# Kernel tuning notes

Hardware: AMD Instinct MI355X
Metric: run time of the kernel (lower is better)

The kernel has to match this reference:

```python
import jax, jax.numpy as jnp
import numpy as np

B, N, E = 64, 512, 262144
D_EMB = 128   # 2 * embedding_dim
D_H = 128     # residue_emb_dim == iegmn_lay_hid_dim
L = 5         # iegmn_n_lays
X_INIT = 0.25 # residual mix toward original coords (IEGMN x_connection_init)


def silu(x):
    return x * jax.nn.sigmoid(x)


def _edges(k):
    # within-graph random edges: pick a graph, then a node inside it
    g = jax.random.randint(k, (E,), 0, B)
    n = jax.random.randint(jax.random.fold_in(k, 1), (E,), 0, N)
    return (g * N + n).astype(jnp.int32)


def setup_inputs() -> dict:
    key = jax.random.key(0)
    ks = jax.random.split(key, 16)
    Nt = B * N
    s = 0.05
    feat = jax.random.normal(ks[0], (Nt, D_EMB), jnp.float32)
    coords = jax.random.normal(ks[1], (Nt, 3), jnp.float32)
    c_valid = (jax.random.uniform(ks[2], (B, N)) > 0.3).astype(jnp.float32)
    c_valid = c_valid.at[:, 0].set(1.0)  # avoid empty graphs
    return {
        'feat': feat,
        'coords': coords,
        'c_valid': c_valid,
        'edge_src': _edges(ks[3]), 'edge_dst': _edges(ks[4]),
        'cross_src': _edges(ks[5]), 'cross_dst': _edges(ks[6]),
        'W_emb': jax.random.normal(ks[7], (D_H, D_EMB), jnp.float32) * s,
        'We1': jax.random.normal(ks[8], (L, 2 * D_H + 1, D_H), jnp.float32) * s,
        'be1': jnp.zeros((L, D_H), jnp.float32),
        'We2': jax.random.normal(ks[9], (L, D_H, D_H), jnp.float32) * s,
        'be2': jnp.zeros((L, D_H), jnp.float32),
        'Wx': jax.random.normal(ks[10], (L, D_H, 1), jnp.float32) * s,
        'Wh': jax.random.normal(ks[11], (L, 3 * D_H, D_H), jnp.float32) * s,
        'bh': jnp.zeros((L, D_H), jnp.float32),
        'Wfc': jax.random.normal(ks[12], (3, D_H, D_H), jnp.float32) * s,
        'bfc': jnp.zeros((3, D_H), jnp.float32),
        'Wout': jax.random.normal(ks[13], (D_H, 1), jnp.float32) * s,
        'bout': jnp.zeros((1,), jnp.float32),
    }


def _deg_inv(dst, n):
    deg = jax.ops.segment_sum(jnp.ones(dst.shape[0], jnp.float32), dst, num_segments=n)
    return (1.0 / jnp.maximum(deg, 1.0))[:, None]


def _iegmn_layer(p, src, dst, x, h, x0, h0, deg_inv):
    We1, be1, We2, be2, Wx, Wh, bh = p
    n = x.shape[0]
    dx = x[src] - x[dst]                                  # [E, 3]
    d2 = jnp.sum(dx * dx, -1, keepdims=True)              # [E, 1]
    m = silu(jnp.concatenate([h[src], h[dst], d2], -1) @ We1 + be1)
    m = silu(m @ We2 + be2)                               # [E, D_H]
    coef = jnp.tanh(m @ Wx)                               # [E, 1]
    agg_x = jax.ops.segment_sum(dx * coef, dst, num_segments=n) * deg_inv
    x_new = X_INIT * x0 + (1.0 - X_INIT) * x + agg_x
    agg_m = jax.ops.segment_sum(m, dst, num_segments=n) * deg_inv
    h_new = silu(jnp.concatenate([h, agg_m, h0], -1) @ Wh + bh)
    return x_new, h_new


def reference(feat, coords, c_valid, edge_src, edge_dst, cross_src, cross_dst,
              W_emb, We1, be1, We2, be2, Wx, Wh, bh, Wfc, bfc, Wout, bout):
    Nt = feat.shape[0]
    h = feat @ W_emb.T          # embede (no bias)
    h0, x0, x = h, coords, coords
    dgi = _deg_inv(edge_dst, Nt)
    dci = _deg_inv(cross_dst, Nt)
    for k in range(L):
        p = tuple(t[k] for t in (We1, be1, We2, be2, Wx, Wh, bh))
        # branch == 'both': run layer on graph then cross_graph with same input h
        x, c1 = _iegmn_layer(p, edge_src, edge_dst, x, h, x0, h0, dgi)
        x, c2 = _iegmn_layer(p, cross_src, cross_dst, x, h, x0, h0, dci)
        h = c2 - c1             # dropout is identity at inference
    # masked sum-pool / count
    hb = h.reshape(B, N, D_H)
    pooled = jnp.sum(hb * c_valid[..., None], axis=1) / jnp.sum(c_valid, axis=1, keepdims=True)
    z = pooled
    for i in range(Wfc.shape[0]):
        z = jax.nn.relu(z @ Wfc[i] + bfc[i])
    out = jax.nn.sigmoid(z @ Wout + bout)
    return out.reshape(-1)      # [B]
```

## Files before the change

### kernel.cpp

```cpp
#include <hip/hip_runtime.h>

#define DEVINL __device__ __forceinline__

constexpr int NT   = 32768;
constexpr int DH   = 128;
constexpr int NE   = 262144;
constexpr int BGR  = 64;
constexpr int NPG  = 512;
constexpr int LAYS = 5;
constexpr size_t LSTR = 32768*3 + 98304;

typedef __attribute__((ext_vector_type(8))) short bf16x8;
typedef __attribute__((ext_vector_type(4))) float f32x4;
typedef __attribute__((ext_vector_type(4))) unsigned int uint4v;
typedef unsigned int uint;

DEVINL float siluf(float v){ return v * (1.0f/(1.0f + __expf(-v))); }
DEVINL float tanh_fast(float x){ float e = __expf(2.0f*x); return 1.0f - 2.0f/(e + 1.0f); }

DEVINL uint bf16_rne(float f){
  uint x = __float_as_uint(f);
  return (x + 0x7fffu + ((x>>16)&1u)) >> 16;
}

DEVINL void split8(const float* m, bf16x8& h, bf16x8& l){
  #pragma unroll
  for (int j=0;j<8;j++){
    uint x  = __float_as_uint(m[j]);
    uint hb = x >> 16;
    float hf = __uint_as_float(hb<<16);
    uint lb = bf16_rne(m[j] - hf);
    h[j] = (short)hb; l[j] = (short)lb;
  }
}

DEVINL f32x4 mma3(bf16x8 ah, bf16x8 al, bf16x8 bh, bf16x8 bl, f32x4 acc){
  acc = __builtin_amdgcn_mfma_f32_16x16x32_bf16(al, bh, acc, 0,0,0);
  acc = __builtin_amdgcn_mfma_f32_16x16x32_bf16(ah, bl, acc, 0,0,0);
  acc = __builtin_amdgcn_mfma_f32_16x16x32_bf16(ah, bh, acc, 0,0,0);
  return acc;
}

__global__ __launch_bounds__(256) void k_prep_all(
    const float* __restrict__ W_emb, const float* __restrict__ We1,
    const float* __restrict__ We2,  const float* __restrict__ Wh,
    short* __restrict__ wemb_p, short* __restrict__ lay_p)
{
  const int idx = blockIdx.x*256 + threadIdx.x;
  const float* src; short* dst; int v; bool trans = false;
  if (idx < 16384){ src = W_emb; dst = wemb_p; v = idx; trans = true; }
  else {
    const int u = idx - 16384;
    const int layer = u / 98304;
    const int w = u - layer*98304;
    short* p = lay_p + (size_t)layer*LSTR;
    if (w < 16384)      { src = We1 + (size_t)layer*257*DH;          dst = p;         v = w; }
    else if (w < 32768) { src = We1 + (size_t)layer*257*DH + 128*DH; dst = p + 32768; v = w - 16384; }
    else if (w < 49152) { src = We2 + (size_t)layer*DH*DH;           dst = p + 65536; v = w - 32768; }
    else                { src = Wh  + (size_t)layer*3*DH*DH;         dst = p + 98304; v = w - 49152; }
  }
  const int k = v>>7, col = v&127;
  const float val = trans ? src[(size_t)col*128 + k] : src[(size_t)k*128 + col];
  uint hb = __float_as_uint(val) >> 16;
  float hf = __uint_as_float(hb<<16);
  uint lb = bf16_rne(val - hf);
  const int kc = k>>5, q = (k&31)>>3, j = k&7;
  const size_t o = (size_t)kc*8192 + q*1024 + col*8 + j;
  dst[o]        = (short)hb;
  dst[o + 4096] = (short)lb;
}

__global__ __launch_bounds__(256) void k_hist2(const int* __restrict__ edst,
                                               const int* __restrict__ cdst,
                                               int* __restrict__ cnt){
  const int half = blockIdx.x >= (NE/256);
  const int e = (blockIdx.x - half*(NE/256))*256 + threadIdx.x;
  const int* d = half ? cdst : edst;
  atomicAdd(&cnt[half*NT + d[e]], 1);
}

__global__ __launch_bounds__(1024) void k_scan2(const int* __restrict__ cnt,
                                                int* __restrict__ cur,
                                                float* __restrict__ dinv){
  __shared__ int part[1024];
  const int off = blockIdx.x * NT;
  const int tid = threadIdx.x;
  const int base = tid*32;
  int s = 0;
  for (int i=0;i<32;i++){
    const int c = cnt[off + base + i];
    dinv[off + base + i] = 1.0f / (float)(c > 1 ? c : 1);
    s += c;
  }
  const int own = s;
  part[tid] = s; __syncthreads();
  for (int o=1; o<1024; o<<=1){
    int v = (tid>=o) ? part[tid-o] : 0;
    __syncthreads();
    part[tid] += v;
    __syncthreads();
  }
  int run = part[tid] - own;
  for (int i=0;i<32;i++){ cur[off + base + i] = run; run += cnt[off + base + i]; }
}

__global__ __launch_bounds__(256) void k_scatter2(const int* __restrict__ edst,
                                                  const int* __restrict__ cdst,
                                                  int* __restrict__ cur,
                                                  int* __restrict__ perm){
  const int half = blockIdx.x >= (NE/256);
  const int e = (blockIdx.x - half*(NE/256))*256 + threadIdx.x;
  const int* d = half ? cdst : edst;
  const int p = atomicAdd(&cur[half*NT + d[e]], 1);
  perm[half*NE + p] = e;
}

template<int MODE>
__global__ __launch_bounds__(512) void k_ngemm(
    const float* __restrict__ A0, float* __restrict__ A1, const float* __restrict__ A2,
    const float* __restrict__ dinv, const short* __restrict__ W0, const short* __restrict__ W1,
    const float* __restrict__ bias, const float* __restrict__ c1in,
    float* __restrict__ out0, float* __restrict__ out1)
{
  const int tid = threadIdx.x;
  const int wv = tid>>6, lane = tid&63, c = lane&15, q = lane>>4;
  const int rowt = wv & 3, grp = wv >> 2;
  const int row = blockIdx.x*64 + rowt*16 + c;
  constexpr int KC = (MODE>=2) ? 12 : 4;
  constexpr int TT = (MODE==1) ? 8 : 4;
  float dv = 1.0f;
  if constexpr (MODE>=2) dv = dinv[row];
  const short* Wp = W0;
  if constexpr (MODE==1){ if (grp==1) Wp = W1; }
  f32x4 acc[TT];
  #pragma unroll
  for (int t=0;t<TT;t++){ acc[t][0]=0.f; acc[t][1]=0.f; acc[t][2]=0.f; acc[t][3]=0.f; }

  #pragma unroll
  for (int kc=0; kc<KC; ++kc){
    const float* asrc = A0; float sc = 1.0f;
    if constexpr (MODE>=2){
      if (kc >= 8)      { asrc = A2; }
      else if (kc >= 4) { asrc = A1; sc = dv; }
    }
    const int koff = (kc&3)*32 + q*8;
    float4 v0 = *(const float4*)(asrc + (size_t)row*128 + koff);
    float4 v1 = *(const float4*)(asrc + (size_t)row*128 + koff + 4);
    float m[8] = {v0.x*sc,v0.y*sc,v0.z*sc,v0.w*sc,v1.x*sc,v1.y*sc,v1.z*sc,v1.w*sc};
    bf16x8 ah, al; split8(m, ah, al);
    #pragma unroll
    for (int t=0;t<TT;t++){
      const int tg = (MODE==1) ? t : grp*4 + t;
      const short* fp = Wp + (size_t)kc*8192 + q*1024 + (tg*16 + c)*8;
      bf16x8 bh = *(const bf16x8*)fp;
      bf16x8 bl = *(const bf16x8*)(fp + 4096);
      acc[t] = mma3(ah, al, bh, bl, acc[t]);
    }
  }
  #pragma unroll
  for (int t=0;t<TT;t++){
    const int tg = (MODE==1) ? t : grp*4 + t;
    const int col = tg*16 + c;
    float b0 = 0.f;
    if constexpr (MODE==1){ if (grp==0) b0 = bias[col]; }
    else if constexpr (MODE>=2){ b0 = bias[col]; }
    #pragma unroll
    for (int r=0;r<4;r++){
      const size_t orow = (size_t)blockIdx.x*64 + rowt*16 + q*4 + r;
      float v = acc[t][r];
      if constexpr (MODE==0){
        out0[orow*128 + col] = v; out1[orow*128 + col] = v;
      } else if constexpr (MODE==1){
        if (grp==0) out0[orow*128 + col] = v + b0;
        else        out1[orow*128 + col] = v;
      } else if constexpr (MODE==2){
        out0[orow*128 + col] = siluf(v + b0);
      } else {
        out0[orow*128 + col] = siluf(v + b0) - c1in[orow*128 + col];
      }
    }
  }
  if constexpr (MODE>=2){
    __syncthreads();
    float4 z; z.x=0.f; z.y=0.f; z.z=0.f; z.w=0.f;
    float4* zp = (float4*)(A1 + (size_t)blockIdx.x*64*128);
    #pragma unroll
    for (int i=0;i<4;i++) zp[tid + i*512] = z;
  }
}

__global__ __launch_bounds__(512) void k_edge(
    const int* __restrict__ perm, const int* __restrict__ esrc, const int* __restrict__ edst,
    const float* __restrict__ x,  const float* __restrict__ Aw, const float* __restrict__ Bw,
    const short* __restrict__ w2p, const float* __restrict__ We1_l,
    const float* __restrict__ be2_l, const float* __restrict__ Wx_l,
    float* __restrict__ aggm, float* __restrict__ aggx)
{
  __shared__ __align__(16) short w2t[16384];
  __shared__ __align__(16) float w256s[128];
  __shared__ __align__(16) float wxs[128];
  __shared__ __align__(16) float be2s[128];
  __shared__ float dxs[8][16][3];
  __shared__ int   dsts[8][16];
  const int tid = threadIdx.x;
  const int wv = tid>>6, lane = tid&63, c = lane&15, q = lane>>4;
  if (tid < 128){ w256s[tid]=We1_l[256*128+tid]; wxs[tid]=Wx_l[tid]; be2s[tid]=be2_l[tid]; }
  const int er = wv*16 + c;
  const int eg = perm[blockIdx.x*128 + er];
  const int s  = esrc[eg], d = edst[eg];
  const float dx0 = x[s*3+0]-x[d*3+0];
  const float dx1 = x[s*3+1]-x[d*3+1];
  const float dx2 = x[s*3+2]-x[d*3+2];
  const float d2  = dx0*dx0 + dx1*dx1 + dx2*dx2;
  if (q==0){ dxs[wv][c][0]=dx0; dxs[wv][c][1]=dx1; dxs[wv][c][2]=dx2; dsts[wv][c]=d; }
  f32x4 acc[8];
  #pragma unroll
  for (int t=0;t<8;t++){ acc[t][0]=0.f; acc[t][1]=0.f; acc[t][2]=0.f; acc[t][3]=0.f; }
  const int fo = q*1024 + c*8;
  const float* ap = Aw + (size_t)s*128;
  const float* bp = Bw + (size_t)d*128;
  for (int half=0; half<2; ++half){
    __syncthreads();
    #pragma unroll
    for (int i=0;i<4;i++)
      ((uint4v*)w2t)[tid + i*512] = ((const uint4v*)(w2p + half*16384))[tid + i*512];
    __syncthreads();
    #pragma unroll
    for (int ks=0; ks<2; ++ks){
      const int kb = half*64 + ks*32 + q*8;
      float4 av0 = *(const float4*)(ap+kb), av1 = *(const float4*)(ap+kb+4);
      float4 bv0 = *(const float4*)(bp+kb), bv1 = *(const float4*)(bp+kb+4);
      float4 w0  = *(const float4*)&w256s[kb], w1 = *(const float4*)&w256s[kb+4];
      float m[8];
      m[0]=siluf(av0.x+bv0.x+d2*w0.x); m[1]=siluf(av0.y+bv0.y+d2*w0.y);
      m[2]=siluf(av0.z+bv0.z+d2*w0.z); m[3]=siluf(av0.w+bv0.w+d2*w0.w);
      m[4]=siluf(av1.x+bv1.x+d2*w1.x); m[5]=siluf(av1.y+bv1.y+d2*w1.y);
      m[6]=siluf(av1.z+bv1.z+d2*w1.z); m[7]=siluf(av1.w+bv1.w+d2*w1.w);
      bf16x8 ah, al; split8(m, ah, al);
      #pragma unroll
      for (int t=0;t<8;t++){
        bf16x8 bh = *(const bf16x8*)&w2t[ks*8192 + t*128 + fo];
        bf16x8 bl = *(const bf16x8*)&w2t[ks*8192 + 4096 + t*128 + fo];
        acc[t] = mma3(ah, al, bh, bl, acc[t]);
      }
    }
  }
  float pd[4];
  #pragma unroll
  for (int t=0;t<8;t++){
    const float be = be2s[t*16+c], wx = wxs[t*16+c];
    #pragma unroll
    for (int r=0;r<4;r++){
      float v = siluf(acc[t][r] + be);
      acc[t][r] = v;
      if (t==0) pd[r] = v*wx; else pd[r] += v*wx;
    }
  }
  #pragma unroll
  for (int msk=1; msk<16; msk<<=1){
    #pragma unroll
    for (int r=0;r<4;r++) pd[r] += __shfl_xor(pd[r], msk);
  }
  const int rb = q*4;
  const int rd0 = dsts[wv][rb+0], rd1 = dsts[wv][rb+1];
  const int rd2 = dsts[wv][rb+2], rd3 = dsts[wv][rb+3];
  const bool b1 = (rd1!=rd0), b2 = (rd2!=rd1), b3 = (rd3!=rd2);
  {
    #pragma unroll
    for (int t=0;t<8;t++){
      const int col = t*16 + c;
      float v3 = acc[t][3];
      float v2 = acc[t][2] + (b3 ? 0.f : v3);
      float v1 = acc[t][1] + (b2 ? 0.f : v2);
      float v0 = acc[t][0] + (b1 ? 0.f : v1);
      unsafeAtomicAdd(aggm + (size_t)rd0*128 + col, v0);
      if (b1) unsafeAtomicAdd(aggm + (size_t)rd1*128 + col, v1);
      if (b2) unsafeAtomicAdd(aggm + (size_t)rd2*128 + col, v2);
      if (b3) unsafeAtomicAdd(aggm + (size_t)rd3*128 + col, v3);
    }
  }
  if (c < 3){
    float a0 = dxs[wv][rb+0][c]*tanh_fast(pd[0]);
    float a1 = dxs[wv][rb+1][c]*tanh_fast(pd[1]);
    float a2 = dxs[wv][rb+2][c]*tanh_fast(pd[2]);
    float a3 = dxs[wv][rb+3][c]*tanh_fast(pd[3]);
    float v3 = a3;
    float v2 = a2 + (b3 ? 0.f : v3);
    float v1 = a1 + (b2 ? 0.f : v2);
    float v0 = a0 + (b1 ? 0.f : v1);
    unsafeAtomicAdd(aggx + (size_t)rd0*3 + c, v0);
    if (b1) unsafeAtomicAdd(aggx + (size_t)rd1*3 + c, v1);
    if (b2) unsafeAtomicAdd(aggx + (size_t)rd2*3 + c, v2);
    if (b3) unsafeAtomicAdd(aggx + (size_t)rd3*3 + c, v3);
  }
}

__global__ __launch_bounds__(256) void k_xupd(float* __restrict__ x, const float* __restrict__ x0,
                                              float* __restrict__ aggx,
                                              const float* __restrict__ dinv){
  int i = blockIdx.x*256 + threadIdx.x;
  if (i < NT*3){
    int n = i/3;
    x[i] = 0.25f*x0[i] + 0.75f*x[i] + aggx[i]*dinv[n];
    aggx[i] = 0.f;
  }
}

__global__ __launch_bounds__(512) void k_pool(const float* __restrict__ h,
                                              const float* __restrict__ cvalid,
                                              float* __restrict__ pooled){
  __shared__ float red[4][128];
  __shared__ float redc[4];
  const int b = blockIdx.x, t = threadIdx.x, j = t&127, sl = t>>7;
  float s = 0.f, cf = 0.f;
  for (int n=sl; n<NPG; n+=4){
    const float m = cvalid[b*NPG + n];
    s  += h[((size_t)b*NPG + n)*DH + j] * m;
    cf += m;
  }
  red[sl][j] = s;
  if (j==0) redc[sl] = cf;
  __syncthreads();
  if (t < 128){
    float ss = red[0][t]+red[1][t]+red[2][t]+red[3][t];
    float cc = redc[0]+redc[1]+redc[2]+redc[3];
    pooled[b*DH + t] = ss / cc;
  }
}

__global__ __launch_bounds__(256) void k_mlp(const float* __restrict__ pooled,
                                             const float* __restrict__ Wfc,
                                             const float* __restrict__ bfc,
                                             const float* __restrict__ Wout,
                                             const float* __restrict__ bout,
                                             float* __restrict__ out)
{
  __shared__ __align__(16) float z[64*132];
  __shared__ __align__(16) float wB[128*128];
  const int t = threadIdx.x;
  {
    const int n = t>>2, qq = t&3;
    const float4* p = (const float4*)(pooled + n*DH + qq*32);
    float4* w = (float4*)&z[n*132 + qq*32];
    #pragma unroll
    for (int u=0;u<8;u++) w[u] = p[u];
  }
  const int g = t>>5, lane = t&31, c0 = lane*4;
  for (int l=0;l<3;l++){
    #pragma unroll
    for (int i=0;i<16;i++){
      const int idx = t + i*256;
      ((float4*)wB)[idx] = ((const float4*)(Wfc + (size_t)l*DH*DH))[idx];
    }
    __syncthreads();
    float acc[8][4];
    #pragma unroll
    for (int i=0;i<8;i++){ acc[i][0]=0.f; acc[i][1]=0.f; acc[i][2]=0.f; acc[i][3]=0.f; }
    #pragma unroll 4
    for (int kk=0; kk<128; kk+=4){
      float4 b0=*(const float4*)&wB[(kk+0)*128+c0];
      float4 b1=*(const float4*)&wB[(kk+1)*128+c0];
      float4 b2=*(const float4*)&wB[(kk+2)*128+c0];
      float4 b3=*(const float4*)&wB[(kk+3)*128+c0];
      #pragma unroll
      for (int i=0;i<8;i++){
        float4 a=*(const float4*)&z[(g*8+i)*132 + kk];
        acc[i][0]+=a.x*b0.x+a.y*b1.x+a.z*b2.x+a.w*b3.x;
        acc[i][1]+=a.x*b0.y+a.y*b1.y+a.z*b2.y+a.w*b3.y;
        acc[i][2]+=a.x*b0.z+a.y*b1.z+a.z*b2.z+a.w*b3.z;
        acc[i][3]+=a.x*b0.w+a.y*b1.w+a.z*b2.w+a.w*b3.w;
      }
    }
    __syncthreads();
    #pragma unroll
    for (int i=0;i<8;i++){
      float v0=acc[i][0]+bfc[l*DH+c0+0]; v0 = v0>0.f?v0:0.f;
      float v1=acc[i][1]+bfc[l*DH+c0+1]; v1 = v1>0.f?v1:0.f;
      float v2=acc[i][2]+bfc[l*DH+c0+2]; v2 = v2>0.f?v2:0.f;
      float v3=acc[i][3]+bfc[l*DH+c0+3]; v3 = v3>0.f?v3:0.f;
      float4 v; v.x=v0; v.y=v1; v.z=v2; v.w=v3;
      *(float4*)&z[(g*8+i)*132 + c0] = v;
    }
    __syncthreads();
  }
  if (t < 64){
    float a = 0.f;
    for (int k2=0;k2<128;k2++) a += z[t*132 + k2]*Wout[k2];
    out[t] = 1.0f/(1.0f + __expf(-(a + bout[0])));
  }
}

extern "C" void kernel_launch(void* const* d_in, const int* in_sizes, int n_in,
                              void* d_out, int out_size, void* d_ws, size_t ws_size,
                              hipStream_t stream)
{
  (void)in_sizes; (void)n_in; (void)out_size; (void)ws_size;
  const float* feat   = (const float*)d_in[0];
  const float* coords = (const float*)d_in[1];
  const float* cvalid = (const float*)d_in[2];
  const int*   esrc   = (const int*)d_in[3];
  const int*   edst   = (const int*)d_in[4];
  const int*   csrc   = (const int*)d_in[5];
  const int*   cdst   = (const int*)d_in[6];
  const float* W_emb  = (const float*)d_in[7];
  const float* We1    = (const float*)d_in[8];
  const float* be1    = (const float*)d_in[9];
  const float* We2    = (const float*)d_in[10];
  const float* be2    = (const float*)d_in[11];
  const float* Wx     = (const float*)d_in[12];
  const float* Wh     = (const float*)d_in[13];
  const float* bh     = (const float*)d_in[14];
  const float* Wfc    = (const float*)d_in[15];
  const float* bfc    = (const float*)d_in[16];
  const float* Wout   = (const float*)d_in[17];
  const float* bout   = (const float*)d_in[18];

  float* ws = (float*)d_ws;
  float* h      = ws; ws += (size_t)NT*DH;
  float* h0     = ws; ws += (size_t)NT*DH;
  float* c1     = ws; ws += (size_t)NT*DH;
  float* Aw     = ws; ws += (size_t)NT*DH;
  float* Bw     = ws; ws += (size_t)NT*DH;
  float* aggm   = ws; ws += (size_t)NT*DH;
  float* aggx   = ws; ws += (size_t)NT*3;
  float* x      = ws; ws += (size_t)NT*3;
  float* dgi    = ws; ws += NT;
  float* dci    = ws; ws += NT;
  float* pooled = ws; ws += BGR*DH;
  int* permG  = (int*)ws; ws += NE;
  int* permC  = (int*)ws; ws += NE;
  int* cnt    = (int*)c1;
  int* cursor = cnt + 2*NT;
  short* pst    = (short*)ws;
  short* wemb_p = pst;
  short* lay_p  = pst + 32768;

  hipMemsetAsync(aggm, 0, (size_t)NT*(DH+3)*sizeof(float), stream);

  k_prep_all<<<1984, 256, 0, stream>>>(W_emb, We1, We2, Wh, wemb_p, lay_p);

  hipMemsetAsync(cnt, 0, 2*NT*sizeof(int), stream);
  k_hist2   <<<2*(NE/256), 256, 0, stream>>>(edst, cdst, cnt);
  k_scan2   <<<2, 1024, 0, stream>>>(cnt, cursor, dgi);
  k_scatter2<<<2*(NE/256), 256, 0, stream>>>(edst, cdst, cursor, permG);

  k_ngemm<0><<<NT/64, 512, 0, stream>>>(feat, nullptr, nullptr, nullptr,
                                        wemb_p, nullptr, nullptr, nullptr, h, h0);
  hipMemcpyAsync(x, coords, (size_t)NT*3*sizeof(float), hipMemcpyDeviceToDevice, stream);

  for (int k=0; k<LAYS; k++){
    short* p = lay_p + (size_t)k*LSTR;
    const float* We1_l = We1 + (size_t)k*257*DH;
    const float* be1_l = be1 + (size_t)k*DH;
    const float* be2_l = be2 + (size_t)k*DH;
    const float* Wx_l  = Wx  + (size_t)k*DH;
    const float* bh_l  = bh  + (size_t)k*DH;

    k_ngemm<1><<<NT/64, 512, 0, stream>>>(h, nullptr, nullptr, nullptr,
                                          p, p + 32768, be1_l, nullptr, Aw, Bw);
    k_edge<<<NE/128, 512, 0, stream>>>(permG, esrc, edst, x, Aw, Bw,
                                       p + 65536, We1_l, be2_l, Wx_l, aggm, aggx);
    k_xupd<<<(NT*3+255)/256, 256, 0, stream>>>(x, coords, aggx, dgi);
    k_ngemm<2><<<NT/64, 512, 0, stream>>>(h, aggm, h0, dgi,
                                          p + 98304, nullptr, bh_l, nullptr, c1, nullptr);
    k_edge<<<NE/128, 512, 0, stream>>>(permG + NE, csrc, cdst, x, Aw, Bw,
                                       p + 65536, We1_l, be2_l, Wx_l, aggm, aggx);
    k_xupd<<<(NT*3+255)/256, 256, 0, stream>>>(x, coords, aggx, dci);
    k_ngemm<3><<<NT/64, 512, 0, stream>>>(h, aggm, h0, dci,
                                          p + 98304, nullptr, bh_l, c1, h, nullptr);
  }

  k_pool<<<BGR, 512, 0, stream>>>(h, cvalid, pooled);
  k_mlp <<<1, 256, 0, stream>>>(pooled, Wfc, bfc, Wout, bout, (float*)d_out);
}
```

Baseline: 1.780 ms.

## Pre-sort edge src/dst pairs, load whole W2 to LDS asynchronously, restructure edge kernel

The scatter step now writes sorted (src,dst) int2 pairs, so the edge kernel skips the perm→esrc/edst indirection. The edge kernel loads the full 64KB W2 tile into LDS with one set of direct global-to-LDS loads, replacing two staged halves and their extra barriers. It also prefetches all A/B rows up front and splits the MFMA work into two column groups so fewer accumulators are live. The larger LDS footprint and the launch bound of 4 may reduce occupancy or cause register spills.

```diff
diff --git a/kernel.cpp b/kernel.cpp
--- a/kernel.cpp
+++ b/kernel.cpp
@@ -40,6 +40,10 @@
   acc = __builtin_amdgcn_mfma_f32_16x16x32_bf16(ah, bh, acc, 0,0,0);
   return acc;
 }
+
+#define GLOAD_LDS16(g, l) __builtin_amdgcn_global_load_lds( \
+    (const __attribute__((address_space(1))) void*)(g), \
+    (__attribute__((address_space(3))) void*)(l), 16, 0, 0)
 
 __global__ __launch_bounds__(256) void k_prep_all(
     const float* __restrict__ W_emb, const float* __restrict__ We1,
@@ -104,15 +108,20 @@
   for (int i=0;i<32;i++){ cur[off + base + i] = run; run += cnt[off + base + i]; }
 }
 
-__global__ __launch_bounds__(256) void k_scatter2(const int* __restrict__ edst,
+__global__ __launch_bounds__(256) void k_scatter2(const int* __restrict__ esrc,
+                                                  const int* __restrict__ edst,
+                                                  const int* __restrict__ csrc,
                                                   const int* __restrict__ cdst,
                                                   int* __restrict__ cur,
-                                                  int* __restrict__ perm){
+                                                  int2* __restrict__ sd){
   const int half = blockIdx.x >= (NE/256);
   const int e = (blockIdx.x - half*(NE/256))*256 + threadIdx.x;
-  const int* d = half ? cdst : edst;
-  const int p = atomicAdd(&cur[half*NT + d[e]], 1);
-  perm[half*NE + p] = e;
+  const int* sA = half ? csrc : esrc;
+  const int* dA = half ? cdst : edst;
+  const int dv = dA[e];
+  const int p = atomicAdd(&cur[half*NT + dv], 1);
+  int2 v; v.x = sA[e]; v.y = dv;
+  sd[half*NE + p] = v;
 }
 
 template<int MODE>
@@ -189,14 +198,14 @@
   }
 }
 
-__global__ __launch_bounds__(512) void k_edge(
-    const int* __restrict__ perm, const int* __restrict__ esrc, const int* __restrict__ edst,
-    const float* __restrict__ x,  const float* __restrict__ Aw, const float* __restrict__ Bw,
+__global__ __launch_bounds__(512, 4) void k_edge(
+    const int2* __restrict__ sd, const float* __restrict__ x,
+    const float* __restrict__ Aw, const float* __restrict__ Bw,
     const short* __restrict__ w2p, const float* __restrict__ We1_l,
     const float* __restrict__ be2_l, const float* __restrict__ Wx_l,
     float* __restrict__ aggm, float* __restrict__ aggx)
 {
-  __shared__ __align__(16) short w2t[16384];
+  __shared__ __align__(16) short w2t[32768];
   __shared__ __align__(16) float w256s[128];
   __shared__ __align__(16) float wxs[128];
   __shared__ __align__(16) float be2s[128];
@@ -204,80 +213,90 @@
   __shared__ int   dsts[8][16];
   const int tid = threadIdx.x;
   const int wv = tid>>6, lane = tid&63, c = lane&15, q = lane>>4;
+  const int er = wv*16 + c;
+  const int2 sdv = sd[blockIdx.x*128 + er];
+  #pragma unroll
+  for (int i=0;i<8;i++)
+    GLOAD_LDS16(w2p + (size_t)(tid + i*512)*8, w2t + (size_t)(wv*64 + i*512)*8);
   if (tid < 128){ w256s[tid]=We1_l[256*128+tid]; wxs[tid]=Wx_l[tid]; be2s[tid]=be2_l[tid]; }
-  const int er = wv*16 + c;
-  const int eg = perm[blockIdx.x*128 + er];
-  const int s  = esrc[eg], d = edst[eg];
-  const float dx0 = x[s*3+0]-x[d*3+0];
-  const float dx1 = x[s*3+1]-x[d*3+1];
-  const float dx2 = x[s*3+2]-x[d*3+2];
+  const int s = sdv.x, d = sdv.y;
+  const float xs0=x[s*3+0], xs1=x[s*3+1], xs2=x[s*3+2];
+  const float xd0=x[d*3+0], xd1=x[d*3+1], xd2=x[d*3+2];
+  const float* ap = Aw + (size_t)s*128 + q*8;
+  const float* bp = Bw + (size_t)d*128 + q*8;
+  float4 aa[8], bb[8];
+  #pragma unroll
+  for (int kc=0;kc<4;kc++){
+    aa[2*kc]   = *(const float4*)(ap + kc*32);
+    aa[2*kc+1] = *(const float4*)(ap + kc*32 + 4);
+    bb[2*kc]   = *(const float4*)(bp + kc*32);
+    bb[2*kc+1] = *(const float4*)(bp + kc*32 + 4);
+  }
+  const float dx0 = xs0-xd0, dx1 = xs1-xd1, dx2 = xs2-xd2;
   const float d2  = dx0*dx0 + dx1*dx1 + dx2*dx2;
   if (q==0){ dxs[wv][c][0]=dx0; dxs[wv][c][1]=dx1; dxs[wv][c][2]=dx2; dsts[wv][c]=d; }
-  f32x4 acc[8];
-  #pragma unroll
-  for (int t=0;t<8;t++){ acc[t][0]=0.f; acc[t][1]=0.f; acc[t][2]=0.f; acc[t][3]=0.f; }
-  const int fo = q*1024 + c*8;
-  const float* ap = Aw + (size_t)s*128;
-  const float* bp = Bw + (size_t)d*128;
-  for (int half=0; half<2; ++half){
-    __syncthreads();
-    #pragma unroll
-    for (int i=0;i<4;i++)
-      ((uint4v*)w2t)[tid + i*512] = ((const uint4v*)(w2p + half*16384))[tid + i*512];
-    __syncthreads();
-    #pragma unroll
-    for (int ks=0; ks<2; ++ks){
-      const int kb = half*64 + ks*32 + q*8;
-      float4 av0 = *(const float4*)(ap+kb), av1 = *(const float4*)(ap+kb+4);
-      float4 bv0 = *(const float4*)(bp+kb), bv1 = *(const float4*)(bp+kb+4);
-      float4 w0  = *(const float4*)&w256s[kb], w1 = *(const float4*)&w256s[kb+4];
-      float m[8];
-      m[0]=siluf(av0.x+bv0.x+d2*w0.x); m[1]=siluf(av0.y+bv0.y+d2*w0.y);
-      m[2]=siluf(av0.z+bv0.z+d2*w0.z); m[3]=siluf(av0.w+bv0.w+d2*w0.w);
-      m[4]=siluf(av1.x+bv1.x+d2*w1.x); m[5]=siluf(av1.y+bv1.y+d2*w1.y);
-      m[6]=siluf(av1.z+bv1.z+d2*w1.z); m[7]=siluf(av1.w+bv1.w+d2*w1.w);
-      bf16x8 ah, al; split8(m, ah, al);
-      #pragma unroll
-      for (int t=0;t<8;t++){
-        bf16x8 bh = *(const bf16x8*)&w2t[ks*8192 + t*128 + fo];
-        bf16x8 bl = *(const bf16x8*)&w2t[ks*8192 + 4096 + t*128 + fo];
-        acc[t] = mma3(ah, al, bh, bl, acc[t]);
-      }
-    }
-  }
-  float pd[4];
-  #pragma unroll
-  for (int t=0;t<8;t++){
-    const float be = be2s[t*16+c], wx = wxs[t*16+c];
-    #pragma unroll
-    for (int r=0;r<4;r++){
-      float v = siluf(acc[t][r] + be);
-      acc[t][r] = v;
-      if (t==0) pd[r] = v*wx; else pd[r] += v*wx;
-    }
-  }
-  #pragma unroll
-  for (int msk=1; msk<16; msk<<=1){
-    #pragma unroll
-    for (int r=0;r<4;r++) pd[r] += __shfl_xor(pd[r], msk);
-  }
+  __syncthreads();
+
+  bf16x8 ah[4], al[4];
+  #pragma unroll
+  for (int kc=0;kc<4;kc++){
+    const int kb = kc*32 + q*8;
+    float4 w0 = *(const float4*)&w256s[kb], w1 = *(const float4*)&w256s[kb+4];
+    float4 av0=aa[2*kc], av1=aa[2*kc+1], bv0=bb[2*kc], bv1=bb[2*kc+1];
+    float m[8];
+    m[0]=siluf(av0.x+bv0.x+d2*w0.x); m[1]=siluf(av0.y+bv0.y+d2*w0.y);
+    m[2]=siluf(av0.z+bv0.z+d2*w0.z); m[3]=siluf(av0.w+bv0.w+d2*w0.w);
+    m[4]=siluf(av1.x+bv1.x+d2*w1.x); m[5]=siluf(av1.y+bv1.y+d2*w1.y);
+    m[6]=siluf(av1.z+bv1.z+d2*w1.z); m[7]=siluf(av1.w+bv1.w+d2*w1.w);
+    split8(m, ah[kc], al[kc]);
+  }
+
   const int rb = q*4;
   const int rd0 = dsts[wv][rb+0], rd1 = dsts[wv][rb+1];
   const int rd2 = dsts[wv][rb+2], rd3 = dsts[wv][rb+3];
   const bool b1 = (rd1!=rd0), b2 = (rd2!=rd1), b3 = (rd3!=rd2);
-  {
-    #pragma unroll
-    for (int t=0;t<8;t++){
-      const int col = t*16 + c;
-      float v3 = acc[t][3];
-      float v2 = acc[t][2] + (b3 ? 0.f : v3);
-      float v1 = acc[t][1] + (b2 ? 0.f : v2);
-      float v0 = acc[t][0] + (b1 ? 0.f : v1);
+
+  float pd[4] = {0.f, 0.f, 0.f, 0.f};
+  #pragma unroll
+  for (int gi=0; gi<2; ++gi){
+    f32x4 acc[4];
+    #pragma unroll
+    for (int tt=0;tt<4;tt++){ acc[tt][0]=0.f; acc[tt][1]=0.f; acc[tt][2]=0.f; acc[tt][3]=0.f; }
+    #pragma unroll
+    for (int kc=0;kc<4;kc++){
+      #pragma unroll
+      for (int tt=0;tt<4;tt++){
+        const int col = (gi*4+tt)*16 + c;
+        const short* fp = &w2t[kc*8192 + q*1024 + col*8];
+        bf16x8 bh = *(const bf16x8*)fp;
+        bf16x8 bl = *(const bf16x8*)(fp + 4096);
+        acc[tt] = mma3(ah[kc], al[kc], bh, bl, acc[tt]);
+      }
+    }
+    #pragma unroll
+    for (int tt=0;tt<4;tt++){
+      const int col = (gi*4+tt)*16 + c;
+      const float be = be2s[col], wx = wxs[col];
+      #pragma unroll
+      for (int r=0;r<4;r++){
+        float v = siluf(acc[tt][r] + be);
+        acc[tt][r] = v;
+        pd[r] += v*wx;
+      }
+      float v3 = acc[tt][3];
+      float v2 = acc[tt][2] + (b3 ? 0.f : v3);
+      float v1 = acc[tt][1] + (b2 ? 0.f : v2);
+      float v0 = acc[tt][0] + (b1 ? 0.f : v1);
       unsafeAtomicAdd(aggm + (size_t)rd0*128 + col, v0);
       if (b1) unsafeAtomicAdd(aggm + (size_t)rd1*128 + col, v1);
       if (b2) unsafeAtomicAdd(aggm + (size_t)rd2*128 + col, v2);
       if (b3) unsafeAtomicAdd(aggm + (size_t)rd3*128 + col, v3);
     }
+  }
+  #pragma unroll
+  for (int msk=1; msk<16; msk<<=1){
+    #pragma unroll
+    for (int r=0;r<4;r++) pd[r] += __shfl_xor(pd[r], msk);
   }
   if (c < 3){
     float a0 = dxs[wv][rb+0][c]*tanh_fast(pd[0]);
@@ -427,8 +446,7 @@
   float* dgi    = ws; ws += NT;
   float* dci    = ws; ws += NT;
   float* pooled = ws; ws += BGR*DH;
-  int* permG  = (int*)ws; ws += NE;
-  int* permC  = (int*)ws; ws += NE;
+  int2* sdG   = (int2*)ws; ws += (size_t)4*NE;
   int* cnt    = (int*)c1;
   int* cursor = cnt + 2*NT;
   short* pst    = (short*)ws;
@@ -442,7 +460,7 @@
   hipMemsetAsync(cnt, 0, 2*NT*sizeof(int), stream);
   k_hist2   <<<2*(NE/256), 256, 0, stream>>>(edst, cdst, cnt);
   k_scan2   <<<2, 1024, 0, stream>>>(cnt, cursor, dgi);
-  k_scatter2<<<2*(NE/256), 256, 0, stream>>>(edst, cdst, cursor, permG);
+  k_scatter2<<<2*(NE/256), 256, 0, stream>>>(esrc, edst, csrc, cdst, cursor, sdG);
 
   k_ngemm<0><<<NT/64, 512, 0, stream>>>(feat, nullptr, nullptr, nullptr,
                                         wemb_p, nullptr, nullptr, nullptr, h, h0);
@@ -458,12 +476,12 @@
 
     k_ngemm<1><<<NT/64, 512, 0, stream>>>(h, nullptr, nullptr, nullptr,
                                           p, p + 32768, be1_l, nullptr, Aw, Bw);
-    k_edge<<<NE/128, 512, 0, stream>>>(permG, esrc, edst, x, Aw, Bw,
+    k_edge<<<NE/128, 512, 0, stream>>>(sdG, x, Aw, Bw,
                                        p + 65536, We1_l, be2_l, Wx_l, aggm, aggx);
     k_xupd<<<(NT*3+255)/256, 256, 0, stream>>>(x, coords, aggx, dgi);
     k_ngemm<2><<<NT/64, 512, 0, stream>>>(h, aggm, h0, dgi,
                                           p + 98304, nullptr, bh_l, nullptr, c1, nullptr);
-    k_edge<<<NE/128, 512, 0, stream>>>(permG + NE, csrc, cdst, x, Aw, Bw,
+    k_edge<<<NE/128, 512, 0, stream>>>(sdG + NE, x, Aw, Bw,
                                        p + 65536, We1_l, be2_l, Wx_l, aggm, aggx);
     k_xupd<<<(NT*3+255)/256, 256, 0, stream>>>(x, coords, aggx, dci);
     k_ngemm<3><<<NT/64, 512, 0, stream>>>(h, aggm, h0, dci,
```

Result: faster. 1.724 ms (-3.1%).
